# Kernel optimization log

Hardware: AMD Instinct MI355X
Metric: run time of the kernel (lower is better)

## Reference

```python
import jax, jax.numpy as jnp
import numpy as np

NUM_HEADS = 12
QUERY_SCALE = 0.125  # hard-coded 1/sqrt(64) in the original module


def setup_inputs() -> dict:
    key = jax.random.key(0)
    ks = jax.random.split(key, 5)
    S, B, H = 1024, 8, 768
    return {
        "hidden_states": jax.random.normal(ks[0], (S, B, H), dtype=jnp.float32),
        "in_proj_weight": jax.random.normal(ks[1], (3 * H, H), dtype=jnp.float32) * 0.02,
        "in_proj_bias": jax.random.normal(ks[2], (3 * H,), dtype=jnp.float32) * 0.02,
        "out_proj_weight": jax.random.normal(ks[3], (H, H), dtype=jnp.float32) * 0.02,
        "out_proj_bias": jax.random.normal(ks[4], (H,), dtype=jnp.float32) * 0.02,
    }


def reference(hidden_states, in_proj_weight, in_proj_bias, out_proj_weight, out_proj_bias):
    S, B, H = hidden_states.shape
    h = NUM_HEADS
    d = H // h

    # fused QKV in-projection: (S, B, 3H)
    mixed = hidden_states @ in_proj_weight.T + in_proj_bias
    q, k, v = jnp.split(mixed, 3, axis=-1)
    q = q * QUERY_SCALE

    def to_heads(x):  # (S, B, H) -> (B*h, S, d)
        return x.reshape(S, B * h, d).transpose(1, 0, 2)

    q, k, v = to_heads(q), to_heads(k), to_heads(v)

    scores = jnp.einsum("nsd,ntd->nst", q, k)          # (B*h, S, S)
    probs = jax.nn.softmax(scores, axis=-1)            # dropout is identity in eval
    ctx = jnp.einsum("nst,ntd->nsd", probs, v)         # (B*h, S, d)

    ctx = ctx.transpose(1, 0, 2).reshape(S, B, H)      # back to (S, B, H)
    return ctx @ out_proj_weight.T + out_proj_bias
```

## Files before the change

### kernel.cpp

```cpp
#include <hip/hip_runtime.h>

#define NH 12

typedef __bf16 bf16x8 __attribute__((ext_vector_type(8)));
typedef __bf16 bf16x4 __attribute__((ext_vector_type(4)));
typedef float f32x4 __attribute__((ext_vector_type(4)));

typedef const __attribute__((address_space(1))) void* gas_ptr;
typedef __attribute__((address_space(3))) void* las_ptr;

__device__ __forceinline__ void gload_lds16(const __bf16* g, __bf16* l) {
    __builtin_amdgcn_global_load_lds((gas_ptr)g, (las_ptr)l, 16, 0, 0);
}

#define QSCALE 0.18033688011112042f

__global__ void convert_kernel(const float* __restrict__ hs,
                               const float* __restrict__ w1,
                               const float* __restrict__ w2,
                               __bf16* __restrict__ xh,
                               __bf16* __restrict__ wq,
                               __bf16* __restrict__ wo) {
    const long long C0 = 786432;
    const long long C1 = 221184;
    const long long C2 = 73728;
    long long i = (long long)blockIdx.x * blockDim.x + threadIdx.x;
    const long long stride = (long long)gridDim.x * blockDim.x;
    for (; i < C0 + C1 + C2; i += stride) {
        const float* src; __bf16* dst; long long j;
        if (i < C0)           { src = hs; dst = xh; j = i; }
        else if (i < C0 + C1) { src = w1; dst = wq; j = i - C0; }
        else                  { src = w2; dst = wo; j = i - C0 - C1; }
        f32x4 v0 = *(const f32x4*)(src + j * 8);
        f32x4 v1 = *(const f32x4*)(src + j * 8 + 4);
        bf16x8 o;
#pragma unroll
        for (int r = 0; r < 4; r++) { o[r] = (__bf16)v0[r]; o[4 + r] = (__bf16)v1[r]; }
        *(bf16x8*)(dst + j * 8) = o;
    }
}

template <int MODE, int BM>
__global__ __launch_bounds__(BM * 4) void gemm_nt(
    const __bf16* __restrict__ A, const __bf16* __restrict__ Bm,
    const float* __restrict__ bias,
    __bf16* __restrict__ qb, __bf16* __restrict__ kb, __bf16* __restrict__ vT,
    float* __restrict__ outf, int M, int N, int K, int NXB)
{
    constexpr int THREADS = BM * 4;
    constexpr int ASZ = BM * 64 * 2;
    constexpr int BSZ = 128 * 64 * 2;
    constexpr int BUNITS = 1024 / THREADS;
    constexpr int SMEMSZ = (MODE == 0) ? 66560 : (2 * ASZ + 2 * BSZ);
    __shared__ __align__(16) char SMEM[SMEMSZ];

    const int t = threadIdx.x;
    const int lane = t & 63;
    const int w = t >> 6;
    const int wr = w >> 2, wc = w & 3;
    const int fr = lane & 15, g4 = lane >> 4;

    const int cpx = gridDim.x >> 3;
    const int orig = blockIdx.x;
    int bx, by;
    if constexpr (MODE == 0) {
        const int xcd = orig & 7, idx = orig >> 3;
        const int halfSz = cpx >> 1;
        const int half = idx / halfSz, rem = idx - half * halfSz;
        const int halfN = NXB >> 1;
        by = xcd * (cpx / NXB) + rem / halfN;
        bx = half * halfN + rem % halfN;
    } else {
        const int swz = (orig & 7) * cpx + (orig >> 3);
        bx = swz % NXB; by = swz / NXB;
    }
    const int m0 = by * BM, n0 = bx * 128;

    f32x4 acc[4][2];
    const f32x4 z4 = {0.f, 0.f, 0.f, 0.f};
#pragma unroll
    for (int i = 0; i < 4; i++)
#pragma unroll
        for (int j = 0; j < 2; j++) acc[i][j] = z4;

    const int kSteps = K >> 6;

    auto As_ = [&](int b) { return (__bf16*)(SMEM + b * ASZ); };
    auto Bs_ = [&](int b) { return (__bf16*)(SMEM + 2 * ASZ + b * BSZ); };

    auto stage = [&](int tk, int b) {
#pragma unroll
        for (int u = 0; u < 2; u++) {
            const int c = u * THREADS + t;
            const int row = c >> 3;
            const int cb = ((c & 7) ^ (row & 7)) * 8;
            gload_lds16(A + (size_t)(m0 + row) * K + tk * 64 + cb, As_(b) + c * 8);
        }
#pragma unroll
        for (int u = 0; u < BUNITS; u++) {
            const int c = u * THREADS + t;
            const int row = c >> 3;
            const int cb = ((c & 7) ^ (row & 7)) * 8;
            gload_lds16(Bm + (size_t)(n0 + row) * K + tk * 64 + cb, Bs_(b) + c * 8);
        }
    };

    auto compute = [&](int cur) {
#pragma unroll
        for (int h = 0; h < 2; h++) {
            bf16x8 af[4], bfr[2];
#pragma unroll
            for (int i = 0; i < 4; i++) {
                const int r = wr * 64 + i * 16 + fr;
                af[i] = *(const bf16x8*)&As_(cur)[r * 64 + (((h * 4 + g4) ^ (r & 7)) * 8)];
            }
#pragma unroll
            for (int j = 0; j < 2; j++) {
                const int r = wc * 32 + j * 16 + fr;
                bfr[j] = *(const bf16x8*)&Bs_(cur)[r * 64 + (((h * 4 + g4) ^ (r & 7)) * 8)];
            }
            __builtin_amdgcn_s_setprio(1);
#pragma unroll
            for (int i = 0; i < 4; i++)
#pragma unroll
                for (int j = 0; j < 2; j++)
                    acc[i][j] = __builtin_amdgcn_mfma_f32_16x16x32_bf16(af[i], bfr[j], acc[i][j], 0, 0, 0);
            __builtin_amdgcn_s_setprio(0);
        }
    };

    stage(0, 0);
    __syncthreads();
    int cur = 0;
    for (int ks = 0; ks < kSteps; ks++) {
        if (ks < kSteps - 1) stage(ks + 1, cur ^ 1);
        compute(cur);
        __syncthreads();
        cur ^= 1;
    }

    if constexpr (MODE == 1) {
#pragma unroll
        for (int j = 0; j < 2; j++) {
            const int gc = n0 + wc * 32 + j * 16 + fr;
            const float bv = bias[gc];
#pragma unroll
            for (int i = 0; i < 4; i++)
#pragma unroll
                for (int r = 0; r < 4; r++) {
                    const int gr = m0 + wr * 64 + i * 16 + g4 * 4 + r;
                    outf[(size_t)gr * N + gc] = acc[i][j][r] + bv;
                }
        }
    } else {
        const int which = (n0 >= 1536) ? 2 : (n0 >= 768 ? 1 : 0);
        if (which < 2) {
#pragma unroll
            for (int j = 0; j < 2; j++) {
                const int gc = n0 + wc * 32 + j * 16 + fr;
                const float bv = bias[gc];
                const int jj = gc - which * 768;
                const int head = jj >> 6, dim = jj & 63;
#pragma unroll
                for (int i = 0; i < 4; i++)
#pragma unroll
                    for (int r = 0; r < 4; r++) {
                        const int gr = m0 + wr * 64 + i * 16 + g4 * 4 + r;
                        const int s = gr >> 3, b = gr & 7;
                        const size_t n = (size_t)(b * NH + head);
                        const float val = acc[i][j][r] + bv;
                        if (which == 0) qb[(n * 1024 + s) * 64 + dim] = (__bf16)(val * QSCALE);
                        else            kb[(n * 1024 + s) * 64 + dim] = (__bf16)val;
                    }
            }
        } else {
            float* Cw = (float*)SMEM;
#pragma unroll
            for (int j = 0; j < 2; j++) {
                const int col = wc * 32 + j * 16 + fr;
                const float bv = bias[n0 + col];
#pragma unroll
                for (int i = 0; i < 4; i++)
#pragma unroll
                    for (int r = 0; r < 4; r++) {
                        const int l = wr * 64 + i * 16 + g4 * 4 + r;
                        Cw[l * 130 + col] = acc[i][j][r] + bv;
                    }
            }
            __syncthreads();
            const int hbase = (n0 - 1536) >> 6;
            const int s0 = m0 >> 3;
#pragma unroll
            for (int u = 0; u < 2; u++) {
                const int c = u * THREADS + t;
                const int b = c >> 7;
                const int hd = (c >> 6) & 1;
                const int dim = c & 63;
                const size_t n = (size_t)(b * NH + hbase + hd);
                __bf16* dst = vT + (n * 64 + dim) * 1024 + s0;
                bf16x8 o0, o1;
#pragma unroll
                for (int sl = 0; sl < 8; sl++)
                    o0[sl] = (__bf16)Cw[(sl * 8 + b) * 130 + hd * 64 + dim];
#pragma unroll
                for (int sl = 0; sl < 8; sl++)
                    o1[sl] = (__bf16)Cw[((sl + 8) * 8 + b) * 130 + hd * 64 + dim];
                *(bf16x8*)dst = o0;
                *(bf16x8*)(dst + 8) = o1;
            }
        }
    }
}

__global__ __launch_bounds__(512) void attn_kernel(
    const __bf16* __restrict__ qb, const __bf16* __restrict__ kb,
    const __bf16* __restrict__ vT, __bf16* __restrict__ ctx)
{
    __shared__ __bf16 Kl[2][64 * 64];
    __shared__ __bf16 Vl[2][80 * 64];
    const int t = threadIdx.x, lane = t & 63, w = t >> 6;

    const int orig = blockIdx.x;
    const int swz = (orig & 7) * 96 + (orig >> 3);
    const int n = swz >> 3;
    const int q0 = (swz & 7) * 128;
    const int fr = lane & 15, g4 = lane >> 4;
    const int fx = fr & 7;

    const __bf16* qptr = qb + ((size_t)n * 1024 + q0 + w * 16 + fr) * 64 + g4 * 8;
    const bf16x8 qf0 = *(const bf16x8*)qptr;
    const bf16x8 qf1 = *(const bf16x8*)(qptr + 32);

    float mval = -1e30f;
    const f32x4 z4 = {0.f, 0.f, 0.f, 0.f};
    f32x4 o[5] = {z4, z4, z4, z4, z4};

    const int srow = t >> 3;
    const int scb  = (t & 7) ^ (srow & 7);
    const int tt_s = srow >> 4, rho = srow & 15;
    const int krow = 32 * (tt_s >> 1) + 8 * (rho >> 2) + 4 * (tt_s & 1) + (rho & 3);
    const __bf16* kbase = kb + (size_t)n * 65536;
    const __bf16* vbase = vT + (size_t)n * 65536;

    {
        const int b = t >> 8;
        const int rem = (t * 4) & 1023;
        const int row = 64 + (rem >> 6), col = rem & 63;
        bf16x4 v;
        const __bf16 f = (__bf16)((row == 64) ? 1.0f : 0.0f);
        v[0] = f; v[1] = f; v[2] = f; v[3] = f;
        *(bf16x4*)&Vl[b][row * 64 + col] = v;
    }

    gload_lds16(kbase + (size_t)krow * 64 + scb * 8,   &Kl[0][t * 8]);
    gload_lds16(vbase + (size_t)srow * 1024 + scb * 8, &Vl[0][t * 8]);
    __syncthreads();

    int cur = 0;
    for (int kc = 0; kc < 16; kc++) {
        if (kc < 15) {
            const int t0 = (kc + 1) * 64;
            gload_lds16(kbase + (size_t)(t0 + krow) * 64 + scb * 8,  &Kl[cur ^ 1][t * 8]);
            gload_lds16(vbase + (size_t)srow * 1024 + t0 + scb * 8,  &Vl[cur ^ 1][t * 8]);
        }

        f32x4 sc[4];
        __builtin_amdgcn_s_setprio(1);
#pragma unroll
        for (int tt = 0; tt < 4; tt++) {
            const int row = (tt * 16 + fr) * 64;
            bf16x8 kf0 = *(const bf16x8*)&Kl[cur][row + ((g4 ^ fx) * 8)];
            bf16x8 kf1 = *(const bf16x8*)&Kl[cur][row + (((4 + g4) ^ fx) * 8)];
            f32x4 s = __builtin_amdgcn_mfma_f32_16x16x32_bf16(kf0, qf0, z4, 0, 0, 0);
            s = __builtin_amdgcn_mfma_f32_16x16x32_bf16(kf1, qf1, s, 0, 0, 0);
            sc[tt] = s;
        }
        __builtin_amdgcn_s_setprio(0);

        float a[16];
#pragma unroll
        for (int tt = 0; tt < 4; tt++)
#pragma unroll
            for (int r = 0; r < 4; r++) a[tt * 4 + r] = sc[tt][r];

        const float t0m = fmaxf(fmaxf(a[0],  a[1]),  a[2]);
        const float t1m = fmaxf(fmaxf(a[3],  a[4]),  a[5]);
        const float t2m = fmaxf(fmaxf(a[6],  a[7]),  a[8]);
        const float t3m = fmaxf(fmaxf(a[9],  a[10]), a[11]);
        const float t4m = fmaxf(fmaxf(a[12], a[13]), a[14]);
        float pmax = fmaxf(fmaxf(fmaxf(t0m, t1m), t2m),
                           fmaxf(fmaxf(t3m, t4m), a[15]));
        pmax = fmaxf(pmax, __shfl_xor(pmax, 16));
        pmax = fmaxf(pmax, __shfl_xor(pmax, 32));

        if (pmax > mval + 8.0f) {
            const float sf = __builtin_amdgcn_exp2f(mval - pmax);
#pragma unroll
            for (int dt = 0; dt < 5; dt++) o[dt] *= sf;
            mval = pmax;
        }

        bf16x8 pa0, pa1;
#pragma unroll
        for (int i = 0; i < 8; i++)  pa0[i] = (__bf16)__builtin_amdgcn_exp2f(a[i] - mval);
#pragma unroll
        for (int i = 0; i < 8; i++)  pa1[i] = (__bf16)__builtin_amdgcn_exp2f(a[8 + i] - mval);

        __builtin_amdgcn_s_setprio(1);
#pragma unroll
        for (int ks = 0; ks < 2; ks++) {
            const bf16x8 pa = ks ? pa1 : pa0;
#pragma unroll
            for (int dt = 0; dt < 5; dt++) {
                bf16x8 vf = *(const bf16x8*)&Vl[cur][(dt * 16 + fr) * 64 + (((4 * ks + g4) ^ fx) * 8)];
                o[dt] = __builtin_amdgcn_mfma_f32_16x16x32_bf16(vf, pa, o[dt], 0, 0, 0);
            }
        }
        __builtin_amdgcn_s_setprio(0);

        if (kc < 15) __syncthreads();
        cur ^= 1;
    }

    float lsum = o[4][0];
    lsum += __shfl_xor(lsum, 16);
    lsum += __shfl_xor(lsum, 32);

    const int b = n / NH, head = n % NH;
    const float rl = 1.0f / lsum;
    const int srw = q0 + w * 16 + fr;
    __bf16* cbase = ctx + ((size_t)srw * 8 + b) * 768 + head * 64;
#pragma unroll
    for (int dt = 0; dt < 4; dt++) {
        bf16x4 ov;
#pragma unroll
        for (int r = 0; r < 4; r++) ov[r] = (__bf16)(o[dt][r] * rl);
        *(bf16x4*)&cbase[dt * 16 + g4 * 4] = ov;
    }
}

extern "C" void kernel_launch(void* const* d_in, const int* in_sizes, int n_in,
                              void* d_out, int out_size, void* d_ws, size_t ws_size,
                              hipStream_t stream) {
    const float* hs = (const float*)d_in[0];
    const float* w1 = (const float*)d_in[1];
    const float* b1 = (const float*)d_in[2];
    const float* w2 = (const float*)d_in[3];
    const float* b2 = (const float*)d_in[4];
    float* out = (float*)d_out;

    char* ws = (char*)d_ws;
    __bf16* qb  = (__bf16*)(ws);
    __bf16* kb  = (__bf16*)(ws + 12582912);
    __bf16* vT  = (__bf16*)(ws + 25165824);
    __bf16* Xh  = (__bf16*)(ws + 37748736);
    __bf16* Wq  = (__bf16*)(ws + 50331648);
    __bf16* Wo  = (__bf16*)(ws + 53870592);
    __bf16* Ctx = Xh;

    convert_kernel<<<2048, 256, 0, stream>>>(hs, w1, w2, Xh, Wq, Wo);
    gemm_nt<0, 128><<<1152, 512, 0, stream>>>(Xh, Wq, b1, qb, kb, vT, nullptr, 8192, 2304, 768, 18);
    attn_kernel<<<768, 512, 0, stream>>>(qb, kb, vT, Ctx);
    gemm_nt<1, 64><<<768, 256, 0, stream>>>(Ctx, Wo, b2, nullptr, nullptr, nullptr, out, 8192, 768, 768, 6);
}
```

Measured before the change: 105.6 us.

## Process two query tiles per wave in attention to reuse K/V fragments

The attention kernel now uses 4 waves (256 threads) per block instead of 8, and each wave handles 32 query rows as two 16-row tiles. Each K and V fragment read from LDS feeds two MFMAs, which halves LDS read traffic per unit of math and gives more independent MFMA chains. Each thread now issues two async global-to-LDS loads per stage. The cost is higher register pressure from doubled accumulators and fewer waves per block to hide latency.

Result: slower. 112.7 us (+6.8%).

```diff
diff --git a/kernel.cpp b/kernel.cpp
--- a/kernel.cpp
+++ b/kernel.cpp
@@ -212,7 +212,7 @@
     }
 }
 
-__global__ __launch_bounds__(512) void attn_kernel(
+__global__ __launch_bounds__(256) void attn_kernel(
     const __bf16* __restrict__ qb, const __bf16* __restrict__ kb,
     const __bf16* __restrict__ vT, __bf16* __restrict__ ctx)
 {
@@ -227,93 +227,138 @@
     const int fr = lane & 15, g4 = lane >> 4;
     const int fx = fr & 7;
 
-    const __bf16* qptr = qb + ((size_t)n * 1024 + q0 + w * 16 + fr) * 64 + g4 * 8;
-    const bf16x8 qf0 = *(const bf16x8*)qptr;
-    const bf16x8 qf1 = *(const bf16x8*)(qptr + 32);
-
-    float mval = -1e30f;
+    const __bf16* qbase = qb + ((size_t)n * 1024 + q0 + w * 32 + fr) * 64 + g4 * 8;
+    const bf16x8 qf00 = *(const bf16x8*)qbase;
+    const bf16x8 qf01 = *(const bf16x8*)(qbase + 32);
+    const bf16x8 qf10 = *(const bf16x8*)(qbase + 16 * 64);
+    const bf16x8 qf11 = *(const bf16x8*)(qbase + 16 * 64 + 32);
+
+    float mval0 = -1e30f, mval1 = -1e30f;
     const f32x4 z4 = {0.f, 0.f, 0.f, 0.f};
-    f32x4 o[5] = {z4, z4, z4, z4, z4};
-
-    const int srow = t >> 3;
-    const int scb  = (t & 7) ^ (srow & 7);
-    const int tt_s = srow >> 4, rho = srow & 15;
-    const int krow = 32 * (tt_s >> 1) + 8 * (rho >> 2) + 4 * (tt_s & 1) + (rho & 3);
+    f32x4 o0[5] = {z4, z4, z4, z4, z4};
+    f32x4 o1[5] = {z4, z4, z4, z4, z4};
+
+    int krowA[2], vrowA[2], scbA[2], lofsA[2];
+#pragma unroll
+    for (int u = 0; u < 2; u++) {
+        const int c = u * 256 + t;
+        const int row = c >> 3;
+        scbA[u] = ((c & 7) ^ (row & 7)) * 8;
+        lofsA[u] = c * 8;
+        const int tt_s = row >> 4, rho = row & 15;
+        krowA[u] = 32 * (tt_s >> 1) + 8 * (rho >> 2) + 4 * (tt_s & 1) + (rho & 3);
+        vrowA[u] = row;
+    }
     const __bf16* kbase = kb + (size_t)n * 65536;
     const __bf16* vbase = vT + (size_t)n * 65536;
 
     {
-        const int b = t >> 8;
-        const int rem = (t * 4) & 1023;
+        const int b = t >> 7;
+        const int rem = (t & 127) * 8;
         const int row = 64 + (rem >> 6), col = rem & 63;
-        bf16x4 v;
+        bf16x8 v;
         const __bf16 f = (__bf16)((row == 64) ? 1.0f : 0.0f);
-        v[0] = f; v[1] = f; v[2] = f; v[3] = f;
-        *(bf16x4*)&Vl[b][row * 64 + col] = v;
-    }
-
-    gload_lds16(kbase + (size_t)krow * 64 + scb * 8,   &Kl[0][t * 8]);
-    gload_lds16(vbase + (size_t)srow * 1024 + scb * 8, &Vl[0][t * 8]);
+#pragma unroll
+        for (int i = 0; i < 8; i++) v[i] = f;
+        *(bf16x8*)&Vl[b][row * 64 + col] = v;
+    }
+
+#pragma unroll
+    for (int u = 0; u < 2; u++) {
+        gload_lds16(kbase + (size_t)krowA[u] * 64 + scbA[u], &Kl[0][lofsA[u]]);
+        gload_lds16(vbase + (size_t)vrowA[u] * 1024 + scbA[u], &Vl[0][lofsA[u]]);
+    }
     __syncthreads();
 
     int cur = 0;
     for (int kc = 0; kc < 16; kc++) {
         if (kc < 15) {
             const int t0 = (kc + 1) * 64;
-            gload_lds16(kbase + (size_t)(t0 + krow) * 64 + scb * 8,  &Kl[cur ^ 1][t * 8]);
-            gload_lds16(vbase + (size_t)srow * 1024 + t0 + scb * 8,  &Vl[cur ^ 1][t * 8]);
-        }
-
-        f32x4 sc[4];
+#pragma unroll
+            for (int u = 0; u < 2; u++) {
+                gload_lds16(kbase + (size_t)(t0 + krowA[u]) * 64 + scbA[u], &Kl[cur ^ 1][lofsA[u]]);
+                gload_lds16(vbase + (size_t)vrowA[u] * 1024 + t0 + scbA[u], &Vl[cur ^ 1][lofsA[u]]);
+            }
+        }
+
+        f32x4 sc0[4], sc1[4];
         __builtin_amdgcn_s_setprio(1);
 #pragma unroll
         for (int tt = 0; tt < 4; tt++) {
             const int row = (tt * 16 + fr) * 64;
             bf16x8 kf0 = *(const bf16x8*)&Kl[cur][row + ((g4 ^ fx) * 8)];
             bf16x8 kf1 = *(const bf16x8*)&Kl[cur][row + (((4 + g4) ^ fx) * 8)];
-            f32x4 s = __builtin_amdgcn_mfma_f32_16x16x32_bf16(kf0, qf0, z4, 0, 0, 0);
-            s = __builtin_amdgcn_mfma_f32_16x16x32_bf16(kf1, qf1, s, 0, 0, 0);
-            sc[tt] = s;
+            f32x4 s0 = __builtin_amdgcn_mfma_f32_16x16x32_bf16(kf0, qf00, z4, 0, 0, 0);
+            sc0[tt] = __builtin_amdgcn_mfma_f32_16x16x32_bf16(kf1, qf01, s0, 0, 0, 0);
+            f32x4 s1 = __builtin_amdgcn_mfma_f32_16x16x32_bf16(kf0, qf10, z4, 0, 0, 0);
+            sc1[tt] = __builtin_amdgcn_mfma_f32_16x16x32_bf16(kf1, qf11, s1, 0, 0, 0);
         }
         __builtin_amdgcn_s_setprio(0);
 
-        float a[16];
-#pragma unroll
-        for (int tt = 0; tt < 4; tt++)
-#pragma unroll
-            for (int r = 0; r < 4; r++) a[tt * 4 + r] = sc[tt][r];
-
-        const float t0m = fmaxf(fmaxf(a[0],  a[1]),  a[2]);
-        const float t1m = fmaxf(fmaxf(a[3],  a[4]),  a[5]);
-        const float t2m = fmaxf(fmaxf(a[6],  a[7]),  a[8]);
-        const float t3m = fmaxf(fmaxf(a[9],  a[10]), a[11]);
-        const float t4m = fmaxf(fmaxf(a[12], a[13]), a[14]);
-        float pmax = fmaxf(fmaxf(fmaxf(t0m, t1m), t2m),
-                           fmaxf(fmaxf(t3m, t4m), a[15]));
-        pmax = fmaxf(pmax, __shfl_xor(pmax, 16));
-        pmax = fmaxf(pmax, __shfl_xor(pmax, 32));
-
-        if (pmax > mval + 8.0f) {
-            const float sf = __builtin_amdgcn_exp2f(mval - pmax);
-#pragma unroll
-            for (int dt = 0; dt < 5; dt++) o[dt] *= sf;
-            mval = pmax;
-        }
-
-        bf16x8 pa0, pa1;
-#pragma unroll
-        for (int i = 0; i < 8; i++)  pa0[i] = (__bf16)__builtin_amdgcn_exp2f(a[i] - mval);
-#pragma unroll
-        for (int i = 0; i < 8; i++)  pa1[i] = (__bf16)__builtin_amdgcn_exp2f(a[8 + i] - mval);
+        bf16x8 pa00, pa01, pa10, pa11;
+        {
+            float a[16];
+#pragma unroll
+            for (int tt = 0; tt < 4; tt++)
+#pragma unroll
+                for (int r = 0; r < 4; r++) a[tt * 4 + r] = sc0[tt][r];
+            const float t0m = fmaxf(fmaxf(a[0],  a[1]),  a[2]);
+            const float t1m = fmaxf(fmaxf(a[3],  a[4]),  a[5]);
+            const float t2m = fmaxf(fmaxf(a[6],  a[7]),  a[8]);
+            const float t3m = fmaxf(fmaxf(a[9],  a[10]), a[11]);
+            const float t4m = fmaxf(fmaxf(a[12], a[13]), a[14]);
+            float pmax = fmaxf(fmaxf(fmaxf(t0m, t1m), t2m),
+                               fmaxf(fmaxf(t3m, t4m), a[15]));
+            pmax = fmaxf(pmax, __shfl_xor(pmax, 16));
+            pmax = fmaxf(pmax, __shfl_xor(pmax, 32));
+            if (pmax > mval0 + 8.0f) {
+                const float sf = __builtin_amdgcn_exp2f(mval0 - pmax);
+#pragma unroll
+                for (int dt = 0; dt < 5; dt++) o0[dt] *= sf;
+                mval0 = pmax;
+            }
+#pragma unroll
+            for (int i = 0; i < 8; i++) pa00[i] = (__bf16)__builtin_amdgcn_exp2f(a[i] - mval0);
+#pragma unroll
+            for (int i = 0; i < 8; i++) pa01[i] = (__bf16)__builtin_amdgcn_exp2f(a[8 + i] - mval0);
+        }
+        {
+            float a[16];
+#pragma unroll
+            for (int tt = 0; tt < 4; tt++)
+#pragma unroll
+                for (int r = 0; r < 4; r++) a[tt * 4 + r] = sc1[tt][r];
+            const float t0m = fmaxf(fmaxf(a[0],  a[1]),  a[2]);
+            const float t1m = fmaxf(fmaxf(a[3],  a[4]),  a[5]);
+            const float t2m = fmaxf(fmaxf(a[6],  a[7]),  a[8]);
+            const float t3m = fmaxf(fmaxf(a[9],  a[10]), a[11]);
+            const float t4m = fmaxf(fmaxf(a[12], a[13]), a[14]);
+            float pmax = fmaxf(fmaxf(fmaxf(t0m, t1m), t2m),
+                               fmaxf(fmaxf(t3m, t4m), a[15]));
+            pmax = fmaxf(pmax, __shfl_xor(pmax, 16));
+            pmax = fmaxf(pmax, __shfl_xor(pmax, 32));
+            if (pmax > mval1 + 8.0f) {
+                const float sf = __builtin_amdgcn_exp2f(mval1 - pmax);
+#pragma unroll
+                for (int dt = 0; dt < 5; dt++) o1[dt] *= sf;
+                mval1 = pmax;
+            }
+#pragma unroll
+            for (int i = 0; i < 8; i++) pa10[i] = (__bf16)__builtin_amdgcn_exp2f(a[i] - mval1);
+#pragma unroll
+            for (int i = 0; i < 8; i++) pa11[i] = (__bf16)__builtin_amdgcn_exp2f(a[8 + i] - mval1);
+        }
 
         __builtin_amdgcn_s_setprio(1);
 #pragma unroll
         for (int ks = 0; ks < 2; ks++) {
-            const bf16x8 pa = ks ? pa1 : pa0;
+            const bf16x8 p0 = ks ? pa01 : pa00;
+            const bf16x8 p1 = ks ? pa11 : pa10;
 #pragma unroll
             for (int dt = 0; dt < 5; dt++) {
                 bf16x8 vf = *(const bf16x8*)&Vl[cur][(dt * 16 + fr) * 64 + (((4 * ks + g4) ^ fx) * 8)];
-                o[dt] = __builtin_amdgcn_mfma_f32_16x16x32_bf16(vf, pa, o[dt], 0, 0, 0);
+                o0[dt] = __builtin_amdgcn_mfma_f32_16x16x32_bf16(vf, p0, o0[dt], 0, 0, 0);
+                o1[dt] = __builtin_amdgcn_mfma_f32_16x16x32_bf16(vf, p1, o1[dt], 0, 0, 0);
             }
         }
         __builtin_amdgcn_s_setprio(0);
@@ -322,20 +367,26 @@
         cur ^= 1;
     }
 
-    float lsum = o[4][0];
-    lsum += __shfl_xor(lsum, 16);
-    lsum += __shfl_xor(lsum, 32);
+    float ls0 = o0[4][0];
+    ls0 += __shfl_xor(ls0, 16);
+    ls0 += __shfl_xor(ls0, 32);
+    float ls1 = o1[4][0];
+    ls1 += __shfl_xor(ls1, 16);
+    ls1 += __shfl_xor(ls1, 32);
 
     const int b = n / NH, head = n % NH;
-    const float rl = 1.0f / lsum;
-    const int srw = q0 + w * 16 + fr;
-    __bf16* cbase = ctx + ((size_t)srw * 8 + b) * 768 + head * 64;
+    const float rl0 = 1.0f / ls0;
+    const float rl1 = 1.0f / ls1;
+    const int srw = q0 + w * 32 + fr;
+    __bf16* cb0 = ctx + ((size_t)srw * 8 + b) * 768 + head * 64;
+    __bf16* cb1 = ctx + ((size_t)(srw + 16) * 8 + b) * 768 + head * 64;
 #pragma unroll
     for (int dt = 0; dt < 4; dt++) {
-        bf16x4 ov;
-#pragma unroll
-        for (int r = 0; r < 4; r++) ov[r] = (__bf16)(o[dt][r] * rl);
-        *(bf16x4*)&cbase[dt * 16 + g4 * 4] = ov;
+        bf16x4 ov0, ov1;
+#pragma unroll
+        for (int r = 0; r < 4; r++) { ov0[r] = (__bf16)(o0[dt][r] * rl0); ov1[r] = (__bf16)(o1[dt][r] * rl1); }
+        *(bf16x4*)&cb0[dt * 16 + g4 * 4] = ov0;
+        *(bf16x4*)&cb1[dt * 16 + g4 * 4] = ov1;
     }
 }
 
@@ -360,6 +411,6 @@
 
     convert_kernel<<<2048, 256, 0, stream>>>(hs, w1, w2, Xh, Wq, Wo);
     gemm_nt<0, 128><<<1152, 512, 0, stream>>>(Xh, Wq, b1, qb, kb, vT, nullptr, 8192, 2304, 768, 18);
-    attn_kernel<<<768, 512, 0, stream>>>(qb, kb, vT, Ctx);
+    attn_kernel<<<768, 256, 0, stream>>>(qb, kb, vT, Ctx);
     gemm_nt<1, 64><<<768, 256, 0, stream>>>(Ctx, Wo, b2, nullptr, nullptr, nullptr, out, 8192, 768, 768, 6);
 }
```
